# Kernel tuning notes

Hardware: AMD Instinct MI355X
Metric: run time of the kernel (lower is better)

## Reference

```python
import jax, jax.numpy as jnp
import numpy as np

Y0 = 0.28209479177387814  # Y_0^0 spherical harmonic (degree-0 basis)
CUTOFF = 4.6
K_COUL = 0.529
ENERGY_STD = 1.0
HEADS = 8
N, E, C, L, MID = 32768, 524288, 16, 4, 32
KC = C // 2  # channels_div = 2 -> key/value channels


def _radial(ef, W1, b1, W2, b2, W3, b3):
    # radial profile MLP producing per-edge conv weights
    h = jax.nn.relu(ef @ W1 + b1)
    h = jax.nn.relu(h @ W2 + b2)
    return h @ W3 + b3


def _conv_msg(x_src, ef, bscale, W1, b1, W2, b2, W3, b3, c_out, c_in):
    # degree-0 tensor-field conv: per-edge weight matrix times source feats, times basis
    R = _radial(ef, W1, b1, W2, b2, W3, b3).reshape(-1, c_out, c_in)
    return jnp.einsum('eoi,ei->eo', R, x_src) * bscale[:, None]


def _forward(species, src, dst, rel_pos, emb, kv_W1, kv_b1, kv_W2, kv_b2, kv_W3, kv_b3, Wq, Wproj, fin_W1, fin_b1, fin_W2, fin_b2, fin_W3, fin_b3, Wself, mlp_W1, mlp_b1, mlp_W2, mlp_b2, mlp_W3, mlp_b3):
    n = species.shape[0]
    dist = jnp.linalg.norm(rel_pos, axis=1)
    xc = dist / CUTOFF
    in_cut = dist < CUTOFF
    x2 = jnp.minimum(jnp.where(in_cut, xc * xc, 0.0), 1.0 - 1e-6)
    scale = jnp.where(in_cut, jnp.exp(3.0 - 3.0 / (1.0 - x2)), 0.0)  # bump_fn k=3
    bscale = Y0 * scale  # basis scaled by cutoff envelope per edge
    semb = emb[species - 1]          # [N,C]
    x = semb                         # degree-0 node feats
    # edge feats: (C-1) zero radial-basis channels + distance
    ef = jnp.concatenate([jnp.zeros((dist.shape[0], C - 1), dist.dtype), dist[:, None]], axis=1)
    dh = KC // HEADS
    for l in range(kv_W1.shape[0]):
        kv = _conv_msg(x[src], ef, bscale, kv_W1[l], kv_b1[l], kv_W2[l], kv_b2[l], kv_W3[l], kv_b3[l], 2 * KC, C)
        val, key_ = kv[:, :KC], kv[:, KC:]
        q = x @ Wq[l].T              # [N,KC]
        logits = jnp.einsum('ehd,ehd->eh', key_.reshape(-1, HEADS, dh), q[dst].reshape(-1, HEADS, dh)) / np.sqrt(dh)
        mx = jax.ops.segment_max(logits, dst, num_segments=n)
        w = scale[:, None] * jnp.exp(logits - mx[dst])   # weighted edge softmax
        denom = jax.ops.segment_sum(w, dst, num_segments=n)
        attn = w / jnp.maximum(denom[dst], 1e-20)
        z = (attn[:, :, None] * val.reshape(-1, HEADS, dh)).reshape(-1, KC)
        agg = jax.ops.segment_sum(z, dst, num_segments=n)
        x = jnp.concatenate([agg, x], axis=1) @ Wproj[l].T  # project(cat(attn_out, skip))
        ef = ef + x[src]             # edge feature update via copy_u
    m = _conv_msg(x[src], ef, bscale, fin_W1, fin_b1, fin_W2, fin_b2, fin_W3, fin_b3, C, C)
    feats = jax.ops.segment_sum(m, dst, num_segments=n) + x @ Wself.T  # pooled conv + self-interaction
    cat = jnp.concatenate([semb, feats], axis=1)
    h = jax.nn.silu(cat @ mlp_W1 + mlp_b1)
    h = jax.nn.silu(h @ mlp_W2 + mlp_b2)
    learned = (h @ mlp_W3 + mlp_b3)[:, 0]
    Z = species.astype(dist.dtype)
    Zu, Zv = Z[src], Z[dst]
    raw = K_COUL * Zu * Zv / (2.0 * dist)
    au = 0.8854 * 0.529 / (Zu ** 0.23 + Zv ** 0.23)
    xx = dist / au
    screen = (0.1818 * jnp.exp(-3.2 * xx) + 0.5099 * jnp.exp(-0.9423 * xx)
              + 0.2802 * jnp.exp(-0.4028 * xx) + 0.02817 * jnp.exp(-0.2016 * xx))
    coul = jax.ops.segment_sum(raw * screen * scale, dst, num_segments=n) / ENERGY_STD
    atom_e = (learned + coul) * ENERGY_STD
    return jnp.sum(atom_e)  # SumPooling over a single graph, forces=False


def setup_inputs() -> dict:
    key = jax.random.key(0)
    ks = jax.random.split(key, 32)
    species = jax.random.randint(ks[0], (N,), 1, 90, dtype=jnp.int32)
    src = jax.random.randint(ks[1], (E,), 0, N, dtype=jnp.int32)
    dst = jax.random.randint(ks[2], (E,), 0, N, dtype=jnp.int32)
    d = jax.random.normal(ks[3], (E, 3))
    d = d / jnp.linalg.norm(d, axis=1, keepdims=True)
    r = jax.random.uniform(ks[4], (E, 1), minval=0.5, maxval=5.5)
    rel_pos = (d * r).astype(jnp.float32)
    g = lambda k, sh, fan: (jax.random.normal(k, sh) / np.sqrt(fan)).astype(jnp.float32)
    return dict(
        species=species, src=src, dst=dst, rel_pos=rel_pos,
        emb=g(ks[5], (100, C), 1),
        kv_W1=g(ks[6], (L, C, MID), C), kv_b1=jnp.zeros((L, MID), jnp.float32),
        kv_W2=g(ks[7], (L, MID, MID), MID), kv_b2=jnp.zeros((L, MID), jnp.float32),
        kv_W3=g(ks[8], (L, MID, 2 * KC * C), MID), kv_b3=jnp.zeros((L, 2 * KC * C), jnp.float32),
        Wq=g(ks[9], (L, KC, C), C),
        Wproj=g(ks[10], (L, C, KC + C), KC + C),
        fin_W1=g(ks[11], (C, MID), C), fin_b1=jnp.zeros((MID,), jnp.float32),
        fin_W2=g(ks[12], (MID, MID), MID), fin_b2=jnp.zeros((MID,), jnp.float32),
        fin_W3=g(ks[13], (MID, C * C), MID), fin_b3=jnp.zeros((C * C,), jnp.float32),
        Wself=g(ks[14], (C, C), C),
        mlp_W1=g(ks[15], (2 * C, C), 2 * C), mlp_b1=jnp.zeros((C,), jnp.float32),
        mlp_W2=g(ks[16], (C, C), C), mlp_b2=jnp.zeros((C,), jnp.float32),
        mlp_W3=g(ks[17], (C, 1), C), mlp_b3=jnp.zeros((1,), jnp.float32),
    )


def reference(species, src, dst, rel_pos, emb, kv_W1, kv_b1, kv_W2, kv_b2, kv_W3, kv_b3, Wq, Wproj, fin_W1, fin_b1, fin_W2, fin_b2, fin_W3, fin_b3, Wself, mlp_W1, mlp_b1, mlp_W2, mlp_b2, mlp_W3, mlp_b3):
    return _forward(species, src, dst, rel_pos, emb, kv_W1, kv_b1, kv_W2, kv_b2, kv_W3, kv_b3, Wq, Wproj, fin_W1, fin_b1, fin_W2, fin_b2, fin_W3, fin_b3, Wself, mlp_W1, mlp_b1, mlp_W2, mlp_b2, mlp_W3, mlp_b3)
```

## Files before the change

kernel.cpp:

```cpp
#include <hip/hip_runtime.h>

constexpr float F_Y0     = 0.28209479177387814f;
constexpr float F_CUTOFF = 4.6f;

typedef short short8 __attribute__((ext_vector_type(8)));
typedef float f32x4  __attribute__((ext_vector_type(4)));
typedef float float2v __attribute__((ext_vector_type(2)));

__device__ __forceinline__ float siluf(float v) { return v / (1.0f + __expf(-v)); }

__device__ __forceinline__ unsigned pk2(float a, float b) {
  unsigned r;
  asm("v_cvt_pk_bf16_f32 %0, %1, %2" : "=v"(r) : "v"(a), "v"(b));
  return r;
}
__device__ __forceinline__ float xbf(unsigned d, int h) {
  return __uint_as_float(h ? (d & 0xffff0000u) : (d << 16));
}
__device__ __forceinline__ float2v pkmul2(float2v a, float2v b) {
  float2v d;
  asm("v_pk_mul_f32 %0, %1, %2" : "=v"(d) : "v"(a), "v"(b));
  return d;
}

union FragU { uint4 u; short8 s; };

__device__ __forceinline__ void load16(const float* p, float* r) {
  const float4* p4 = (const float4*)p;
#pragma unroll
  for (int i = 0; i < 4; i++) {
    float4 t = p4[i];
    r[4*i] = t.x; r[4*i+1] = t.y; r[4*i+2] = t.z; r[4*i+3] = t.w;
  }
}
__device__ __forceinline__ void store16(float* p, const float* r) {
  float4* p4 = (float4*)p;
#pragma unroll
  for (int i = 0; i < 4; i++) p4[i] = make_float4(r[4*i], r[4*i+1], r[4*i+2], r[4*i+3]);
}

__device__ __forceinline__ void block_reduce_store(float v, float* part) {
  __shared__ float sred[4];
  int tid = threadIdx.x;
#pragma unroll
  for (int off = 32; off > 0; off >>= 1) v += __shfl_down(v, off, 64);
  if ((tid & 63) == 0) sred[tid >> 6] = v;
  __syncthreads();
  if (tid == 0) part[blockIdx.x] = sred[0] + sred[1] + sred[2] + sred[3];
}

__global__ __launch_bounds__(256) void k_pre(
    const int* __restrict__ species, const int* __restrict__ src, const int* __restrict__ dst,
    const float* __restrict__ rel_pos,
    float* __restrict__ dist_, float* __restrict__ scale_,
    int* __restrict__ cnt,
    float* __restrict__ coul_part,
    int* __restrict__ srcP, float* __restrict__ distP, float* __restrict__ scaleP, int E)
{
  __shared__ float zpow[128];
  int tid = threadIdx.x;
  if (tid < 128) zpow[tid] = __powf((float)tid, 0.23f);
  __syncthreads();

  int e = blockIdx.x * 256 + tid;
  float ce = 0.0f;
  if (e < E) {
    float px = rel_pos[3*(size_t)e + 0];
    float py = rel_pos[3*(size_t)e + 1];
    float pz = rel_pos[3*(size_t)e + 2];
    float dist = sqrtf(px*px + py*py + pz*pz);
    float xc = dist * (1.0f / F_CUTOFF);
    bool in_cut = dist < F_CUTOFF;
    float x2 = in_cut ? xc * xc : 0.0f;
    x2 = fminf(x2, 1.0f - 1e-6f);
    float sc = in_cut ? __expf(3.0f - 3.0f / (1.0f - x2)) : 0.0f;
    dist_[e] = dist;
    scale_[e] = sc;
    srcP[e]   = 0;
    distP[e]  = 1.0f;
    scaleP[e] = 0.0f;
    if (sc > 0.0f) {
      atomicAdd(&cnt[dst[e]], 1);
      int spu = species[src[e]], spv = species[dst[e]];
      float Zu = (float)spu;
      float Zv = (float)spv;
      float raw = 0.529f * Zu * Zv / (2.0f * dist);
      float au = 0.8854f * 0.529f / (zpow[spu] + zpow[spv]);
      float xx = dist / au;
      float screen = 0.1818f   * __expf(-3.2f    * xx)
                   + 0.5099f   * __expf(-0.9423f * xx)
                   + 0.2802f   * __expf(-0.4028f * xx)
                   + 0.02817f  * __expf(-0.2016f * xx);
      ce = raw * screen * sc;
    }
  }
  block_reduce_store(ce, coul_part);
}

__global__ __launch_bounds__(256) void k_scan1(
    const int* __restrict__ cnt, int* __restrict__ row_ptr, int* __restrict__ bsum)
{
  __shared__ int s[256];
  int tid = threadIdx.x;
  int n = blockIdx.x * 256 + tid;
  int v = cnt[n];
  s[tid] = v;
  __syncthreads();
#pragma unroll
  for (int off = 1; off < 256; off <<= 1) {
    int t = (tid >= off) ? s[tid - off] : 0;
    __syncthreads();
    s[tid] += t;
    __syncthreads();
  }
  row_ptr[n] = s[tid] - v;
  if (tid == 255) bsum[blockIdx.x] = s[255];
}

__global__ __launch_bounds__(128) void k_scan2(int* __restrict__ bsum, int* __restrict__ boff)
{
  __shared__ int s[128];
  int tid = threadIdx.x;
  int v = bsum[tid];
  s[tid] = v;
  __syncthreads();
#pragma unroll
  for (int off = 1; off < 128; off <<= 1) {
    int t = (tid >= off) ? s[tid - off] : 0;
    __syncthreads();
    s[tid] += t;
    __syncthreads();
  }
  boff[tid] = s[tid] - v;
}

__global__ __launch_bounds__(256) void k_scan3(
    int* __restrict__ row_ptr, int* __restrict__ row_cur,
    const int* __restrict__ boff, const int* __restrict__ cnt, int N)
{
  int n = blockIdx.x * 256 + threadIdx.x;
  int rp = row_ptr[n] + boff[blockIdx.x];
  row_ptr[n] = rp;
  row_cur[n] = rp;
  if (n == N - 1) row_ptr[N] = rp + cnt[n];
}

__global__ __launch_bounds__(256) void k_scatter_perm(
    const int* __restrict__ dst, const float* __restrict__ scale_,
    int* __restrict__ row_cur,
    int* __restrict__ perm, int E)
{
  int e = blockIdx.x * 256 + threadIdx.x;
  if (e >= E) return;
  if (scale_[e] > 0.0f) {
    int pos = atomicAdd(&row_cur[dst[e]], 1);
    perm[pos] = e;
  }
}

__global__ __launch_bounds__(256) void k_permute(
    const int* __restrict__ perm,
    const int* __restrict__ src, const float* __restrict__ dist_, const float* __restrict__ scale_,
    int* __restrict__ srcP, float* __restrict__ distP, float* __restrict__ scaleP,
    const int* __restrict__ eactp)
{
  int i = blockIdx.x * 256 + threadIdx.x;
  if (i >= eactp[0]) return;
  int e = perm[i];
  srcP[i]   = src[e];
  distP[i]  = dist_[e];
  scaleP[i] = scale_[e];
}

__global__ __launch_bounds__(256) void k_prepack(
    const float* __restrict__ kv_W3, const float* __restrict__ kv_b3,
    const float* __restrict__ fin_W3, const float* __restrict__ fin_b3,
    const float* __restrict__ kv_W2, const float* __restrict__ fin_W2,
    const float* __restrict__ kv_W1, const float* __restrict__ fin_W1,
    uint4* __restrict__ WF)
{
  int t = blockIdx.x * 256 + threadIdx.x;
  if (t >= 5 * 21 * 64) return;
  int lyr = t / (21 * 64);
  int rem = t - lyr * 21 * 64;
  int f = rem >> 6;
  int l = rem & 63;
  int qq = l >> 4;
  int o = l & 15;
  const float* W3 = (lyr < 4) ? (kv_W3 + (size_t)lyr * 32 * 256) : fin_W3;
  const float* B3 = (lyr < 4) ? (kv_b3 + (size_t)lyr * 256) : fin_b3;
  const float* W2 = (lyr < 4) ? (kv_W2 + (size_t)lyr * 32 * 32) : fin_W2;
  const float* W1 = (lyr < 4) ? (kv_W1 + (size_t)lyr * 16 * 32) : fin_W1;
  float v[8];
#pragma unroll
  for (int j = 0; j < 8; j++) {
    if (f < 16) {
      int kk = f * 32 + qq * 8 + j;
      int m = kk >> 4, i = kk & 15;
      v[j] = W3[m * 256 + o * 16 + i];
    } else if (f == 16) {
      int r = qq * 8 + j;
      int mp = r >> 4, i = r & 15;
      v[j] = mp ? 0.0f : B3[o * 16 + i];
    } else if (f < 19) {
      int c = f - 17;
      int p = qq * 8 + j;
      int m = (p & 1) ? (16 + (p >> 1)) : (p >> 1);
      v[j] = W2[m * 32 + c * 16 + o];
    } else {
      int c = f - 19;
      int k = qq * 8 + j;
      v[j] = (k < 16) ? W1[k * 32 + c * 16 + o] : 0.0f;
    }
  }
  uint4 dw;
  dw.x = pk2(v[0], v[1]);
  dw.y = pk2(v[2], v[3]);
  dw.z = pk2(v[4], v[5]);
  dw.w = pk2(v[6], v[7]);
  WF[t] = dw;
}

__global__ __launch_bounds__(256) void k_node_init(
    const int* __restrict__ species, const float* __restrict__ emb,
    const float* __restrict__ Wq0,
    float* __restrict__ x, float* __restrict__ q, int N)
{
  int n = blockIdx.x * 256 + threadIdx.x;
  if (n >= N) return;
  int sp = species[n] - 1;
  float xv[16];
  load16(emb + (size_t)sp * 16, xv);
  store16(x + (size_t)n * 16, xv);
  float qv[8];
#pragma unroll
  for (int h = 0; h < 8; h++) {
    float a = 0.f;
#pragma unroll
    for (int i = 0; i < 16; i++) a += Wq0[h * 16 + i] * xv[i];
    qv[h] = a;
  }
  float4* qp = (float4*)(q + (size_t)n * 8);
  qp[0] = make_float4(qv[0], qv[1], qv[2], qv[3]);
  qp[1] = make_float4(qv[4], qv[5], qv[6], qv[7]);
}

template <int MODE>
__global__ __launch_bounds__(256, 7) void k_edge_conv(
    const int* __restrict__ srcP,
    const float* __restrict__ scaleP, const float* __restrict__ distP,
    const float* __restrict__ xsum, const float* __restrict__ x,
    const float* __restrict__ W1, const float* __restrict__ B1,
    const float* __restrict__ B2,
    const uint4* __restrict__ WF,
    unsigned* __restrict__ kvB, const int* __restrict__ eactp)
{
  if (blockIdx.x * 64 >= eactp[0]) return;
  __shared__ unsigned smem[4 * 1344];
  int tid = threadIdx.x;
  int w = __builtin_amdgcn_readfirstlane(tid >> 6);
  int l = tid & 63;
  int quad = l >> 4;
  int lo = l & 15;
  unsigned* WS  = smem + w * 1344;
  unsigned* P   = WS;
  float*    xsS = (float*)WS;
  unsigned* xsB = WS + 320;
  unsigned* efB = WS + 512;
  unsigned* h1P = WS + 704;
  unsigned* h2P = WS + 1024;

  int ebw = blockIdx.x * 64 + w * 16;

  float b2a = B2[lo], b2b = B2[16 + lo];
  float scv[4];
#pragma unroll
  for (int r = 0; r < 4; r++) scv[r] = scaleP[ebw + quad * 4 + r];

  {
    int e4 = l >> 2, c4 = l & 3;
    int s4 = srcP[ebw + e4];
    float4 xv4 = ((const float4*)(x + (size_t)s4 * 16))[c4];
    float4 ev4;
    if (MODE == 2) {
      ev4 = ((const float4*)(xsum + (size_t)s4 * 16))[c4];
      if (c4 == 3) ev4.w += distP[ebw + e4];
    }
    *(float4*)&xsS[e4 * 20 + c4 * 4] = xv4;
    uint2 xp; xp.x = pk2(xv4.x, xv4.y); xp.y = pk2(xv4.z, xv4.w);
    *(uint2*)&xsB[e4 * 12 + c4 * 2] = xp;
    if (MODE == 2) {
      uint2 ep; ep.x = pk2(ev4.x, ev4.y); ep.y = pk2(ev4.z, ev4.w);
      *(uint2*)&efB[e4 * 12 + c4 * 2] = ep;
    }
  }

  if (MODE == 0) {
    float dd = distP[ebw + lo];
#pragma unroll
    for (int jj = 0; jj < 4; jj++) {
      int d = quad * 4 + jj;
      float v0 = fmaxf(B1[d]      + dd * W1[15 * 32 + d],      0.f);
      float v1 = fmaxf(B1[d + 16] + dd * W1[15 * 32 + d + 16], 0.f);
      h1P[lo * 20 + d] = pk2(v0, v1);
    }
  } else {
    float b1a = B1[lo], b1b = B1[16 + lo];
    FragU a, b0, b1;
    uint4 r = *(const uint4*)&efB[lo * 12 + (quad & 1) * 4];
    uint4 z = make_uint4(0, 0, 0, 0);
    a.u = (quad >= 2) ? z : r;
    b0.u = WF[19 * 64 + l];
    b1.u = WF[20 * 64 + l];
    f32x4 c0 = {0.f, 0.f, 0.f, 0.f};
    f32x4 c1 = {0.f, 0.f, 0.f, 0.f};
    c0 = __builtin_amdgcn_mfma_f32_16x16x32_bf16(a.s, b0.s, c0, 0, 0, 0);
    c1 = __builtin_amdgcn_mfma_f32_16x16x32_bf16(a.s, b1.s, c1, 0, 0, 0);
#pragma unroll
    for (int r2 = 0; r2 < 4; r2++)
      h1P[(quad * 4 + r2) * 20 + lo] =
          pk2(fmaxf(c0[r2] + b1a, 0.f), fmaxf(c1[r2] + b1b, 0.f));
  }

  {
    FragU a, b0, b1;
    a.u = *(const uint4*)&h1P[lo * 20 + quad * 4];
    b0.u = WF[17 * 64 + l];
    b1.u = WF[18 * 64 + l];
    f32x4 hc0 = {0.f, 0.f, 0.f, 0.f};
    f32x4 hc1 = {0.f, 0.f, 0.f, 0.f};
    hc0 = __builtin_amdgcn_mfma_f32_16x16x32_bf16(a.s, b0.s, hc0, 0, 0, 0);
    hc1 = __builtin_amdgcn_mfma_f32_16x16x32_bf16(a.s, b1.s, hc1, 0, 0, 0);
#pragma unroll
    for (int r = 0; r < 4; r++)
      h2P[(quad * 4 + r) * 20 + lo] =
          pk2(fmaxf(hc0[r] + b2a, 0.f), fmaxf(hc1[r] + b2b, 0.f));
  }

  float2v xs2[8];
  {
    const float4* xr = (const float4*)&xsS[lo * 20];
#pragma unroll
    for (int i = 0; i < 4; i++) {
      float4 t = xr[i];
      float2v a; a.x = t.x; a.y = t.y;
      float2v b; b.x = t.z; b.y = t.w;
      xs2[2 * i]     = a;
      xs2[2 * i + 1] = b;
    }
  }
  uint2 hA = *(const uint2*)&h2P[lo * 20 + quad * 2];
  uint2 hB = *(const uint2*)&h2P[lo * 20 + 8 + quad * 2];
  float hmv[8];
  hmv[0] = xbf(hA.x, 0); hmv[1] = xbf(hA.y, 0);
  hmv[2] = xbf(hB.x, 0); hmv[3] = xbf(hB.y, 0);
  hmv[4] = xbf(hA.x, 1); hmv[5] = xbf(hA.y, 1);
  hmv[6] = xbf(hB.x, 1); hmv[7] = xbf(hB.y, 1);

  f32x4 acc = {0.f, 0.f, 0.f, 0.f};
  {
    FragU a, b;
    uint4 r = *(const uint4*)&xsB[lo * 12 + (quad & 1) * 4];
    uint4 z = make_uint4(0, 0, 0, 0);
    a.u = (quad >= 2) ? z : r;
    b.u = WF[16 * 64 + l];
    acc = __builtin_amdgcn_mfma_f32_16x16x32_bf16(a.s, b.s, acc, 0, 0, 0);
  }

#pragma unroll
  for (int q = 0; q < 4; q++) {
#pragma unroll
    for (int j = 0; j < 2; j++) {
      float hm = hmv[q * 2 + j];
      float2v hm2; hm2.x = hm; hm2.y = hm;
      uint4 d0, d1;
      float2v p0 = pkmul2(hm2, xs2[0]);
      float2v p1 = pkmul2(hm2, xs2[1]);
      float2v p2 = pkmul2(hm2, xs2[2]);
      float2v p3 = pkmul2(hm2, xs2[3]);
      d0.x = pk2(p0.x, p0.y); d0.y = pk2(p1.x, p1.y);
      d0.z = pk2(p2.x, p2.y); d0.w = pk2(p3.x, p3.y);
      float2v p4 = pkmul2(hm2, xs2[4]);
      float2v p5 = pkmul2(hm2, xs2[5]);
      float2v p6 = pkmul2(hm2, xs2[6]);
      float2v p7 = pkmul2(hm2, xs2[7]);
      d1.x = pk2(p4.x, p4.y); d1.y = pk2(p5.x, p5.y);
      d1.z = pk2(p6.x, p6.y); d1.w = pk2(p7.x, p7.y);
      int cb = quad * 4 + j * 2;
      *(uint4*)&P[lo * 64 + (((cb)     ^ lo) << 2)] = d0;
      *(uint4*)&P[lo * 64 + (((cb + 1) ^ lo) << 2)] = d1;
    }
#pragma unroll
    for (int t = 0; t < 4; t++) {
      FragU a, b;
      a.u = *(const uint4*)&P[lo * 64 + (((t * 4 + quad) ^ lo) << 2)];
      b.u = WF[(q * 4 + t) * 64 + l];
      acc = __builtin_amdgcn_mfma_f32_16x16x32_bf16(a.s, b.s, acc, 0, 0, 0);
    }
  }

#pragma unroll
  for (int r = 0; r < 4; r++) {
    int e = quad * 4 + r;
    ((float*)h2P)[e * 20 + lo] = acc[r] * (F_Y0 * scv[r]);
  }
  {
    int e2 = l >> 2, c = l & 3;
    const float* row = (const float*)&h2P[e2 * 20 + c * 4];
    float4 t = *(const float4*)row;
    uint2 pkd;
    pkd.x = pk2(t.x, t.y);
    pkd.y = pk2(t.z, t.w);
    *(uint2*)(kvB + ((size_t)(ebw + e2) * 8 + c * 2)) = pkd;
  }
}

template <bool INIT>
__global__ __launch_bounds__(256) void k_agg_update(
    const int* __restrict__ row_ptr, const float* __restrict__ scaleP,
    const unsigned* __restrict__ kvB, const float* __restrict__ qin,
    const float* __restrict__ xin,
    const float* __restrict__ Wproj, const float* __restrict__ Wq_next,
    float* __restrict__ xout, float* __restrict__ qout, float* __restrict__ xsum, int N)
{
  __shared__ float sA[16 * 8];
  __shared__ float sX[16 * 17];
  __shared__ float sN[16 * 17];
  int tid = threadIdx.x;
  int nl = tid >> 4;
  int t16 = tid & 15;
  int h = t16 & 7;
  int p = t16 >> 3;
  int n = blockIdx.x * 16 + nl;
  int hd = h >> 1, hh = h & 1;

  float qh = qin[(size_t)n * 8 + h];
  int j0 = row_ptr[n], j1 = row_ptr[n + 1];
  float num = 0.f, den = 0.f;
  int j = j0 + p;
  for (; j + 6 < j1; j += 8) {
    unsigned va = kvB[(size_t)j * 8 + hd];
    unsigned ka = kvB[(size_t)j * 8 + 4 + hd];
    unsigned vb = kvB[(size_t)(j + 2) * 8 + hd];
    unsigned kb = kvB[(size_t)(j + 2) * 8 + 4 + hd];
    unsigned vc = kvB[(size_t)(j + 4) * 8 + hd];
    unsigned kc = kvB[(size_t)(j + 4) * 8 + 4 + hd];
    unsigned vd = kvB[(size_t)(j + 6) * 8 + hd];
    unsigned kd = kvB[(size_t)(j + 6) * 8 + 4 + hd];
    float sa = scaleP[j];
    float sb = scaleP[j + 2];
    float sc = scaleP[j + 4];
    float sd = scaleP[j + 6];
    float wa = sa * __expf(fminf(xbf(ka, hh) * qh, 60.0f));
    float wb = sb * __expf(fminf(xbf(kb, hh) * qh, 60.0f));
    float wc = sc * __expf(fminf(xbf(kc, hh) * qh, 60.0f));
    float wd = sd * __expf(fminf(xbf(kd, hh) * qh, 60.0f));
    num += wa * xbf(va, hh) + wb * xbf(vb, hh) + wc * xbf(vc, hh) + wd * xbf(vd, hh);
    den += (wa + wb) + (wc + wd);
  }
  for (; j < j1; j += 2) {
    float val = xbf(kvB[(size_t)j * 8 + hd], hh);
    float key = xbf(kvB[(size_t)j * 8 + 4 + hd], hh);
    float lg = fminf(key * qh, 60.0f);
    float wv = scaleP[j] * __expf(lg);
    num += wv * val;
    den += wv;
  }
  num += __shfl_xor(num, 8, 64);
  den += __shfl_xor(den, 8, 64);
  if (p == 0) sA[nl * 8 + h] = num / fmaxf(den, 1e-20f);
  sX[nl * 17 + t16] = xin[(size_t)n * 16 + t16];
  __syncthreads();

  float cat[24];
#pragma unroll
  for (int jj = 0; jj < 8; jj++) cat[jj] = sA[nl * 8 + jj];
#pragma unroll
  for (int jj = 0; jj < 16; jj++) cat[8 + jj] = sX[nl * 17 + jj];
  float xn = 0.f;
#pragma unroll
  for (int jj = 0; jj < 24; jj++) xn += Wproj[t16 * 24 + jj] * cat[jj];
  xout[(size_t)n * 16 + t16] = xn;
  if (INIT) {
    xsum[(size_t)n * 16 + t16] = xn;
  } else {
    xsum[(size_t)n * 16 + t16] += xn;
  }
  sN[nl * 17 + t16] = xn;
  __syncthreads();

  if (p == 0) {
    float a = 0.f;
#pragma unroll
    for (int i = 0; i < 16; i++) a += Wq_next[h * 16 + i] * sN[nl * 17 + i];
    qout[(size_t)n * 8 + h] = a;
  }
}

__global__ __launch_bounds__(256) void k_feats_final(
    const int* __restrict__ row_ptr, const unsigned* __restrict__ kvB,
    const float* __restrict__ x,
    const int* __restrict__ species, const float* __restrict__ emb,
    const float* __restrict__ Wself,
    const float* __restrict__ mW1, const float* __restrict__ mb1,
    const float* __restrict__ mW2, const float* __restrict__ mb2,
    const float* __restrict__ mW3, const float* __restrict__ mb3,
    float* __restrict__ learn_part, int N)
{
  __shared__ float sX[16 * 20];
  __shared__ float sC[16 * 40];
  __shared__ float sH[16 * 20];
  int tid = threadIdx.x;
  int nl = tid >> 4;
  int o = tid & 15;
  int n = blockIdx.x * 16 + nl;
  int od = o >> 1, oh = o & 1;

  int j0 = row_ptr[n], j1 = row_ptr[n + 1];
  float ft = 0.f;
  int j = j0;
  for (; j + 3 < j1; j += 4) {
    unsigned a = kvB[(size_t)j * 8 + od];
    unsigned b = kvB[(size_t)(j + 1) * 8 + od];
    unsigned c = kvB[(size_t)(j + 2) * 8 + od];
    unsigned d = kvB[(size_t)(j + 3) * 8 + od];
    ft += (xbf(a, oh) + xbf(b, oh)) + (xbf(c, oh) + xbf(d, oh));
  }
  for (; j < j1; ++j) ft += xbf(kvB[(size_t)j * 8 + od], oh);

  if (o < 4) {
    float4 v = ((const float4*)(x + (size_t)n * 16))[o];
    *(float4*)&sX[nl * 20 + o * 4] = v;
  } else if (o < 8) {
    int sp = species[n] - 1;
    float4 v = ((const float4*)(emb + (size_t)sp * 16))[o - 4];
    *(float4*)&sC[nl * 40 + (o - 4) * 4] = v;
  }
  __syncthreads();

  float xv[16];
  load16(&sX[nl * 20], xv);
  float a = ft;
#pragma unroll
  for (int i = 0; i < 16; i++) a += Wself[o * 16 + i] * xv[i];
  sC[nl * 40 + 16 + o] = a;
  __syncthreads();

  float cat[32];
  load16(&sC[nl * 40], cat);
  load16(&sC[nl * 40 + 16], cat + 16);
  float hh = mb1[o];
#pragma unroll
  for (int k = 0; k < 32; k++) hh += cat[k] * mW1[k * 16 + o];
  hh = siluf(hh);
  sH[nl * 20 + o] = hh;
  __syncthreads();

  float hv[16];
  load16(&sH[nl * 20], hv);
  float h2 = mb2[o];
#pragma unroll
  for (int k = 0; k < 16; k++) h2 += hv[k] * mW2[k * 16 + o];
  h2 = siluf(h2);
  float contrib = h2 * mW3[o] + ((o == 0) ? mb3[0] : 0.f);
  block_reduce_store(contrib, learn_part);
}

__global__ __launch_bounds__(256) void k_finalize(
    const float* __restrict__ coul_part, int nc,
    const float* __restrict__ learn_part, int nl,
    float* __restrict__ out)
{
  __shared__ float sred[4];
  int tid = threadIdx.x;
  float v = 0.f;
  for (int i = tid; i < nc; i += 256) v += coul_part[i];
  for (int i = tid; i < nl; i += 256) v += learn_part[i];
#pragma unroll
  for (int off = 32; off > 0; off >>= 1) v += __shfl_down(v, off, 64);
  if ((tid & 63) == 0) sred[tid >> 6] = v;
  __syncthreads();
  if (tid == 0) out[0] = sred[0] + sred[1] + sred[2] + sred[3];
}

extern "C" void kernel_launch(void* const* d_in, const int* in_sizes, int n_in,
                              void* d_out, int out_size, void* d_ws, size_t ws_size,
                              hipStream_t stream)
{
  const int*   species = (const int*)d_in[0];
  const int*   src     = (const int*)d_in[1];
  const int*   dst     = (const int*)d_in[2];
  const float* rel_pos = (const float*)d_in[3];
  const float* emb     = (const float*)d_in[4];
  const float* kv_W1   = (const float*)d_in[5];
  const float* kv_b1   = (const float*)d_in[6];
  const float* kv_W2   = (const float*)d_in[7];
  const float* kv_b2   = (const float*)d_in[8];
  const float* kv_W3   = (const float*)d_in[9];
  const float* kv_b3   = (const float*)d_in[10];
  const float* Wq      = (const float*)d_in[11];
  const float* Wproj   = (const float*)d_in[12];
  const float* fin_W1  = (const float*)d_in[13];
  const float* fin_b1  = (const float*)d_in[14];
  const float* fin_W2  = (const float*)d_in[15];
  const float* fin_b2  = (const float*)d_in[16];
  const float* fin_W3  = (const float*)d_in[17];
  const float* fin_b3  = (const float*)d_in[18];
  const float* Wself   = (const float*)d_in[19];
  const float* mlp_W1  = (const float*)d_in[20];
  const float* mlp_b1  = (const float*)d_in[21];
  const float* mlp_W2  = (const float*)d_in[22];
  const float* mlp_b2  = (const float*)d_in[23];
  const float* mlp_W3  = (const float*)d_in[24];
  const float* mlp_b3  = (const float*)d_in[25];

  const int N = in_sizes[0];
  const int E = in_sizes[1];
  const int nblk_e = (E + 255) / 256;
  const int nblk_n = (N + 255) / 256;
  const int nblk_f = N / 16;

  char* p = (char*)d_ws;
  auto alloc = [&](size_t bytes) -> void* {
    void* r = (void*)p;
    p += (bytes + 255) & ~(size_t)255;
    return r;
  };
  float*    dist_   = (float*)alloc((size_t)E * 4);
  float*    scale_  = (float*)alloc((size_t)E * 4);
  float*    distP   = (float*)alloc((size_t)E * 4);
  float*    scaleP  = (float*)alloc((size_t)E * 4);
  int*      srcP    = (int*)  alloc((size_t)E * 4);
  int*      perm    = (int*)  alloc((size_t)E * 4);
  unsigned* kvB     = (unsigned*)alloc((size_t)E * 8 * 4);
  float*    xA      = (float*)alloc((size_t)N * 16 * 4);
  float*    xB      = (float*)alloc((size_t)N * 16 * 4);
  float*    xsum    = (float*)alloc((size_t)N * 16 * 4);
  float*    q       = (float*)alloc((size_t)N * 8 * 4);
  int*      cnt     = (int*)  alloc((size_t)N * 4);
  int*      row_ptr = (int*)  alloc((size_t)(N + 1) * 4);
  int*      row_cur = (int*)  alloc((size_t)N * 4);
  int*      bsum    = (int*)  alloc(128 * 4);
  int*      boff    = (int*)  alloc(128 * 4);
  uint4*    WF      = (uint4*)alloc((size_t)5 * 21 * 64 * 16);
  float*    coul_part  = (float*)alloc((size_t)nblk_e * 4);
  float*    learn_part = (float*)alloc((size_t)nblk_f * 4);

  const int* eactp = row_ptr + N;

  dim3 blk(256);
  dim3 egrid(nblk_e);
  dim3 cgrid(E / 64);
  dim3 ngrid(nblk_n);
  dim3 augrid(N / 16);
  dim3 fgrid(nblk_f);

  hipMemsetAsync(cnt, 0, (size_t)N * 4, stream);

  k_prepack<<<dim3(27), blk, 0, stream>>>(kv_W3, kv_b3, fin_W3, fin_b3,
                                          kv_W2, fin_W2, kv_W1, fin_W1, WF);

  k_pre<<<egrid, blk, 0, stream>>>(species, src, dst, rel_pos, dist_, scale_,
                                   cnt, coul_part, srcP, distP, scaleP, E);
  k_scan1<<<ngrid, blk, 0, stream>>>(cnt, row_ptr, bsum);
  k_scan2<<<dim3(1), dim3(128), 0, stream>>>(bsum, boff);
  k_scan3<<<ngrid, blk, 0, stream>>>(row_ptr, row_cur, boff, cnt, N);
  k_scatter_perm<<<egrid, blk, 0, stream>>>(dst, scale_, row_cur, perm, E);
  k_permute<<<egrid, blk, 0, stream>>>(perm, src, dist_, scale_,
                                       srcP, distP, scaleP, eactp);

  k_node_init<<<ngrid, blk, 0, stream>>>(species, emb, Wq, xA, q, N);

  float* xin = xA;
  float* xout = xB;
  for (int l = 0; l < 4; l++) {
    const float* W1 = kv_W1 + (size_t)l * 16 * 32;
    const float* B1 = kv_b1 + (size_t)l * 32;
    const float* B2 = kv_b2 + (size_t)l * 32;
    const uint4* WFl = WF + (size_t)l * 21 * 64;
    const float* Wqn = Wq + (size_t)((l < 3) ? (l + 1) : 0) * 8 * 16;
    if (l == 0) {
      k_edge_conv<0><<<cgrid, blk, 0, stream>>>(srcP, scaleP, distP, xsum, xin,
                                                W1, B1, B2, WFl, kvB, eactp);
    } else {
      k_edge_conv<2><<<cgrid, blk, 0, stream>>>(srcP, scaleP, distP, xsum, xin,
                                                W1, B1, B2, WFl, kvB, eactp);
    }
    if (l == 0) {
      k_agg_update<true><<<augrid, blk, 0, stream>>>(row_ptr, scaleP, kvB, q, xin,
                                                     Wproj, Wqn, xout, q, xsum, N);
    } else {
      k_agg_update<false><<<augrid, blk, 0, stream>>>(row_ptr, scaleP, kvB, q, xin,
                                                      Wproj + (size_t)l * 16 * 24, Wqn,
                                                      xout, q, xsum, N);
    }
    float* tmp = xin; xin = xout; xout = tmp;
  }

  k_edge_conv<2><<<cgrid, blk, 0, stream>>>(srcP, scaleP, distP, xsum, xin,
                                            fin_W1, fin_b1, fin_b2,
                                            WF + (size_t)4 * 21 * 64, kvB, eactp);
  k_feats_final<<<fgrid, blk, 0, stream>>>(row_ptr, kvB, xin, species, emb, Wself,
                                           mlp_W1, mlp_b1, mlp_W2, mlp_b2, mlp_W3, mlp_b3,
                                           learn_part, N);
  k_finalize<<<dim3(1), blk, 0, stream>>>(coul_part, nblk_e, learn_part, nblk_f,
                                          (float*)d_out);
}
```

Measured before the change: 369.7 us.

## Build outer-product MFMA A-fragments in registers instead of staging through LDS

The h2 activations are now stored in a permuted column order, so each lane can read exactly the hidden values that match its MFMA K-slice. The per-edge outer product of hidden units and source features is then packed straight into the A operand registers. This removes the LDS write/read round trip through the P scratch buffer and halves the per-lane xs register footprint. In exchange it relies on the WF weight fragment order matching the new f-indexed K layout, which is a correctness risk if that packing was not updated.

```diff
diff --git a/kernel.cpp b/kernel.cpp
--- a/kernel.cpp
+++ b/kernel.cpp
@@ -263,7 +263,6 @@
   int quad = l >> 4;
   int lo = l & 15;
   unsigned* WS  = smem + w * 1344;
-  unsigned* P   = WS;
   float*    xsS = (float*)WS;
   unsigned* xsB = WS + 320;
   unsigned* efB = WS + 512;
@@ -331,17 +330,19 @@
     f32x4 hc1 = {0.f, 0.f, 0.f, 0.f};
     hc0 = __builtin_amdgcn_mfma_f32_16x16x32_bf16(a.s, b0.s, hc0, 0, 0, 0);
     hc1 = __builtin_amdgcn_mfma_f32_16x16x32_bf16(a.s, b1.s, hc1, 0, 0, 0);
+    int pp = (lo & 1) * 8 + (lo >> 1);
+    float b2av = b2a, b2bv = b2b;
 #pragma unroll
     for (int r = 0; r < 4; r++)
-      h2P[(quad * 4 + r) * 20 + lo] =
-          pk2(fmaxf(hc0[r] + b2a, 0.f), fmaxf(hc1[r] + b2b, 0.f));
-  }
-
-  float2v xs2[8];
+      h2P[(quad * 4 + r) * 20 + pp] =
+          pk2(fmaxf(hc0[r] + b2av, 0.f), fmaxf(hc1[r] + b2bv, 0.f));
+  }
+
+  float2v xs2[4];
   {
-    const float4* xr = (const float4*)&xsS[lo * 20];
-#pragma unroll
-    for (int i = 0; i < 4; i++) {
+    const float4* xr = (const float4*)&xsS[lo * 20 + (quad & 1) * 8];
+#pragma unroll
+    for (int i = 0; i < 2; i++) {
       float4 t = xr[i];
       float2v a; a.x = t.x; a.y = t.y;
       float2v b; b.x = t.z; b.y = t.w;
@@ -349,13 +350,9 @@
       xs2[2 * i + 1] = b;
     }
   }
-  uint2 hA = *(const uint2*)&h2P[lo * 20 + quad * 2];
-  uint2 hB = *(const uint2*)&h2P[lo * 20 + 8 + quad * 2];
-  float hmv[8];
-  hmv[0] = xbf(hA.x, 0); hmv[1] = xbf(hA.y, 0);
-  hmv[2] = xbf(hB.x, 0); hmv[3] = xbf(hB.y, 0);
-  hmv[4] = xbf(hA.x, 1); hmv[5] = xbf(hA.y, 1);
-  hmv[6] = xbf(hB.x, 1); hmv[7] = xbf(hB.y, 1);
+  uint4 hq0 = *(const uint4*)&h2P[lo * 20 + (quad >> 1) * 8];
+  uint4 hq1 = *(const uint4*)&h2P[lo * 20 + (quad >> 1) * 8 + 4];
+  unsigned hdw[8] = {hq0.x, hq0.y, hq0.z, hq0.w, hq1.x, hq1.y, hq1.z, hq1.w};
 
   f32x4 acc = {0.f, 0.f, 0.f, 0.f};
   {
@@ -368,35 +365,20 @@
   }
 
 #pragma unroll
-  for (int q = 0; q < 4; q++) {
-#pragma unroll
-    for (int j = 0; j < 2; j++) {
-      float hm = hmv[q * 2 + j];
-      float2v hm2; hm2.x = hm; hm2.y = hm;
-      uint4 d0, d1;
-      float2v p0 = pkmul2(hm2, xs2[0]);
-      float2v p1 = pkmul2(hm2, xs2[1]);
-      float2v p2 = pkmul2(hm2, xs2[2]);
-      float2v p3 = pkmul2(hm2, xs2[3]);
-      d0.x = pk2(p0.x, p0.y); d0.y = pk2(p1.x, p1.y);
-      d0.z = pk2(p2.x, p2.y); d0.w = pk2(p3.x, p3.y);
-      float2v p4 = pkmul2(hm2, xs2[4]);
-      float2v p5 = pkmul2(hm2, xs2[5]);
-      float2v p6 = pkmul2(hm2, xs2[6]);
-      float2v p7 = pkmul2(hm2, xs2[7]);
-      d1.x = pk2(p4.x, p4.y); d1.y = pk2(p5.x, p5.y);
-      d1.z = pk2(p6.x, p6.y); d1.w = pk2(p7.x, p7.y);
-      int cb = quad * 4 + j * 2;
-      *(uint4*)&P[lo * 64 + (((cb)     ^ lo) << 2)] = d0;
-      *(uint4*)&P[lo * 64 + (((cb + 1) ^ lo) << 2)] = d1;
-    }
-#pragma unroll
-    for (int t = 0; t < 4; t++) {
-      FragU a, b;
-      a.u = *(const uint4*)&P[lo * 64 + (((t * 4 + quad) ^ lo) << 2)];
-      b.u = WF[(q * 4 + t) * 64 + l];
-      acc = __builtin_amdgcn_mfma_f32_16x16x32_bf16(a.s, b.s, acc, 0, 0, 0);
-    }
+  for (int f = 0; f < 16; f++) {
+    float hm = xbf(hdw[f & 7], f >> 3);
+    float2v hm2; hm2.x = hm; hm2.y = hm;
+    float2v p0 = pkmul2(hm2, xs2[0]);
+    float2v p1 = pkmul2(hm2, xs2[1]);
+    float2v p2 = pkmul2(hm2, xs2[2]);
+    float2v p3 = pkmul2(hm2, xs2[3]);
+    FragU a, b;
+    a.u.x = pk2(p0.x, p0.y);
+    a.u.y = pk2(p1.x, p1.y);
+    a.u.z = pk2(p2.x, p2.y);
+    a.u.w = pk2(p3.x, p3.y);
+    b.u = WF[f * 64 + l];
+    acc = __builtin_amdgcn_mfma_f32_16x16x32_bf16(a.s, b.s, acc, 0, 0, 0);
   }
 
 #pragma unroll
```

After: 361.0 us. 2.4% less time.
